# Kernel optimization log

Hardware: AMD Instinct MI355X
Metric: run time of the kernel (lower is better)

Reference implementation:

```python
import jax, jax.numpy as jnp
import numpy as np
import math

PHI = (1 + math.sqrt(5)) / 2
TABLE_SIZE = 4096
TWO_PI = 2.0 * math.pi
_ang = np.arange(TABLE_SIZE, dtype=np.float32) * (TWO_PI / TABLE_SIZE)
SIN_T = jnp.asarray(np.sin(_ang))
COS_T = jnp.asarray(np.cos(_ang))


def lookup_sin_cos(theta):
    """LUT sin/cos with linear interpolation over a 4096-entry table on [0, 2pi)."""
    pos = (theta / TWO_PI % 1.0) * TABLE_SIZE
    i0f = jnp.floor(pos)
    frac = pos - i0f
    i0 = i0f.astype(jnp.int32) % TABLE_SIZE
    i1 = (i0 + 1) % TABLE_SIZE
    s = SIN_T[i0] * (1.0 - frac) + SIN_T[i1] * frac
    c = COS_T[i0] * (1.0 - frac) + COS_T[i1] * frac
    return s, c


def setup_inputs() -> dict:
    key = jax.random.key(0)
    ks = jax.random.split(key, 8)
    B, S, D, H = 2, 2048, 1024, 16
    dh = D // H
    return {
        "x": jax.random.normal(ks[0], (B, S, D), dtype=jnp.float32),
        "w_q": jax.random.normal(ks[1], (H, dh), dtype=jnp.float32) * 0.02,
        "b_q": jnp.zeros((H, dh), jnp.float32),
        "phi_q": jnp.full((H, dh), PHI, jnp.float32),
        "w_k": jax.random.normal(ks[2], (H, dh), dtype=jnp.float32) * 0.02,
        "b_k": jnp.zeros((H, dh), jnp.float32),
        "phi_k": jnp.full((H, dh), PHI, jnp.float32),
        "w_v": jax.random.normal(ks[3], (H, dh), dtype=jnp.float32) * 0.02,
        "b_v": jnp.zeros((H, dh), jnp.float32),
        "w_out": jax.random.normal(ks[4], (D,), dtype=jnp.float32) * 0.02,
        "b_out": jnp.zeros((D,), jnp.float32),
    }


def reference(x, w_q, b_q, phi_q, w_k, b_k, phi_k, w_v, b_v, w_out, b_out):
    B, S, D = x.shape
    H, dh = w_q.shape
    scale = math.sqrt(2 * dh)
    t = jnp.arange(S, dtype=x.dtype).reshape(1, S, 1, 1)
    xh = x.reshape(B, S, H, dh)

    theta_q = xh / (1.0 + jnp.abs(w_q)) + b_q + t * phi_q
    sin_q, cos_q = lookup_sin_cos(theta_q)
    Q = jnp.concatenate([cos_q, sin_q], axis=-1)  # (B,S,H,2dh)

    theta_k = xh / (1.0 + jnp.abs(w_k)) + b_k + t * phi_k
    sin_k, cos_k = lookup_sin_cos(theta_k)
    K = jnp.concatenate([cos_k, sin_k], axis=-1)  # (B,S,H,2dh)

    theta_v = xh / (1.0 + jnp.abs(w_v)) + b_v
    sin_v, cos_v = lookup_sin_cos(theta_v)
    V = cos_v + sin_v  # (B,S,H,dh)

    scores = jnp.einsum('bqhd,bkhd->bhqk', Q, K) / scale
    causal = jnp.triu(jnp.ones((S, S), dtype=bool), k=1)
    scores = jnp.where(causal, -jnp.inf, scores)
    attn = jax.nn.softmax(scores, axis=-1)
    out = jnp.einsum('bhqk,bkhd->bqhd', attn, V).reshape(B, S, D)

    theta_out = out / (1.0 + jnp.abs(w_out)) + b_out
    sin_o, cos_o = lookup_sin_cos(theta_out)
    return cos_o + sin_o
```

## Files before the change

### kernel.cpp

```cpp
#include <hip/hip_runtime.h>
#include <hip/hip_bf16.h>
#include <math.h>

#define BB 2
#define SS 2048
#define HH 16
#define DH 64
#define DQK 128
#define DD (HH*DH)
#define QSCALE 0.08838834764831845f

typedef _Float16 half8_t __attribute__((ext_vector_type(8)));
typedef float f32x4_t __attribute__((ext_vector_type(4)));
typedef float f32x4v __attribute__((ext_vector_type(4)));

__device__ __forceinline__ void fsincos(float th, float* sn, float* cs) {
  float rev = th * 0.15915494309189535f;
  rev -= floorf(rev);
  float ang = rev * 6.283185307179586f;
  *sn = __sinf(ang);
  *cs = __cosf(ang);
}

__device__ __forceinline__ void dma16(const void* g, void* l) {
  __builtin_amdgcn_global_load_lds(
      (const __attribute__((address_space(1))) unsigned int*)g,
      (__attribute__((address_space(3))) unsigned int*)l, 16, 0, 0);
}

__global__ __launch_bounds__(256) void gen_qkv(
    const float* __restrict__ x,
    const float* __restrict__ wq, const float* __restrict__ bq,
    const float* __restrict__ phq,
    const float* __restrict__ wk, const float* __restrict__ bk,
    const float* __restrict__ phk,
    const float* __restrict__ wv, const float* __restrict__ bv,
    _Float16* __restrict__ Qd, _Float16* __restrict__ Kd, _Float16* __restrict__ Vtd)
{
  int stile = blockIdx.x & 31;
  int bh    = blockIdx.x >> 5;
  int b = bh >> 4, h = bh & 15;
  int t = threadIdx.x;
  int sl = t >> 2;
  int dq = (t & 3) << 4;
  int s  = stile * 64 + sl;

  __shared__ _Float16 Vl[64 * 65];

  const float* xr = x + (((size_t)b * SS + s) * HH + h) * DH + dq;
  float xv[16];
#pragma unroll
  for (int i = 0; i < 4; i++)
    *(f32x4v*)(&xv[i * 4]) = *(const f32x4v*)(xr + i * 4);

  float tv = (float)s;
  _Float16 qc[16], qs[16], kc[16], ks[16];
#pragma unroll
  for (int i = 0; i < 16; i++) {
    int d = dq + i;
    int hd = h * DH + d;
    {
      float th = xv[i] / (1.f + fabsf(wq[hd])) + bq[hd] + tv * phq[hd];
      float sn, cs; fsincos(th, &sn, &cs);
      qc[i] = (_Float16)(cs * QSCALE);
      qs[i] = (_Float16)(sn * QSCALE);
    }
    {
      float th = xv[i] / (1.f + fabsf(wk[hd])) + bk[hd] + tv * phk[hd];
      float sn, cs; fsincos(th, &sn, &cs);
      kc[i] = (_Float16)cs;
      ks[i] = (_Float16)sn;
    }
    {
      float th = xv[i] / (1.f + fabsf(wv[hd])) + bv[hd];
      float sn, cs; fsincos(th, &sn, &cs);
      Vl[d * 65 + sl] = (_Float16)(cs + sn);
    }
  }
  size_t qbase = ((size_t)bh * SS + s) * DQK;
#pragma unroll
  for (int i = 0; i < 2; i++) {
    *(half8_t*)(Qd + qbase + dq + i * 8)      = *(half8_t*)(&qc[i * 8]);
    *(half8_t*)(Qd + qbase + DH + dq + i * 8) = *(half8_t*)(&qs[i * 8]);
  }
  {
    size_t ktb = ((size_t)bh * 32 + stile) * 8192;
    int fo0 = (t & 3) * 2;
    *(half8_t*)(Kd + ktb + ((size_t)(fo0    ) * 64 + sl) * 8) = *(half8_t*)(&kc[0]);
    *(half8_t*)(Kd + ktb + ((size_t)(fo0 + 1) * 64 + sl) * 8) = *(half8_t*)(&kc[8]);
    *(half8_t*)(Kd + ktb + ((size_t)(fo0 + 8) * 64 + sl) * 8) = *(half8_t*)(&ks[0]);
    *(half8_t*)(Kd + ktb + ((size_t)(fo0 + 9) * 64 + sl) * 8) = *(half8_t*)(&ks[8]);
  }
  __syncthreads();
#pragma unroll
  for (int i = 0; i < 2; i++) {
    int u = t * 2 + i;
    int dv = u & 63, ku = u >> 6;
    _Float16 tmp[8];
#pragma unroll
    for (int jj = 0; jj < 8; jj++) tmp[jj] = Vl[dv * 65 + ku * 8 + jj];
    *(half8_t*)(Vtd + (((size_t)bh * 32 + stile) * 8 + ku) * 512 + dv * 8) =
        *(half8_t*)tmp;
  }
}

__global__ __launch_bounds__(256) void flash_attn(
    const _Float16* __restrict__ Qd, const _Float16* __restrict__ Kd,
    const _Float16* __restrict__ Vtd,
    const float* __restrict__ wout, const float* __restrict__ bout,
    float* __restrict__ out)
{
  int j  = blockIdx.x & 15;
  int bh = blockIdx.x >> 4;
  int wave = threadIdx.x >> 6;
  int lane = threadIdx.x & 63;
  int lm = lane & 15, lq = lane >> 4;
  int qh = wave >> 1;
  int kh = wave & 1;

  __shared__ __align__(16) _Float16 KV[2][12288];
  __shared__ __align__(16) _Float16 Pbuf[4][32 * 36];

  const _Float16* Kg = Kd + (size_t)bh * 32 * 8192;
  const _Float16* Vg = Vtd + (size_t)bh * 32 * 4096;
  _Float16* Pw = &Pbuf[wave][0];

  for (int phase = 0; phase < 2; ++phase) {
    int qt = phase == 0 ? (31 - j) : j;
    int nch = qt + 1;
    int q0 = qt * 64;

    __syncthreads();

    const _Float16* Qb = Qd + ((size_t)bh * SS + q0 + qh * 32) * DQK;
    half8_t aq[2][4];
#pragma unroll
    for (int mt = 0; mt < 2; mt++)
#pragma unroll
      for (int c = 0; c < 4; c++)
        aq[mt][c] = *(const half8_t*)(Qb + (mt * 16 + lm) * DQK + c * 32 + lq * 8);

    f32x4_t o[2][4];
    float l[2][4];
#pragma unroll
    for (int mt = 0; mt < 2; mt++) {
#pragma unroll
      for (int nt4 = 0; nt4 < 4; nt4++) o[mt][nt4] = (f32x4_t){0.f, 0.f, 0.f, 0.f};
#pragma unroll
      for (int r = 0; r < 4; r++) l[mt][r] = 0.f;
    }

    {
#pragma unroll
      for (int i = 0; i < 4; i++)
        dma16(Kg + (size_t)(wave * 4 + i) * 512 + lane * 8, &KV[0][(wave * 4 + i) * 512]);
#pragma unroll
      for (int i = 0; i < 2; i++)
        dma16(Vg + (size_t)(wave * 2 + i) * 512 + lane * 8, &KV[0][8192 + (wave * 2 + i) * 512]);
    }

    for (int kt = 0; kt < nch; ++kt) {
      int bf = kt & 1;
      asm volatile("s_waitcnt vmcnt(0)" ::: "memory");
      __syncthreads();
      if (kt + 1 < nch) {
        int nb = (kt + 1) & 1;
        const _Float16* gK = Kg + (size_t)(kt + 1) * 8192;
        const _Float16* gV = Vg + (size_t)(kt + 1) * 4096;
#pragma unroll
        for (int i = 0; i < 4; i++)
          dma16(gK + (size_t)(wave * 4 + i) * 512 + lane * 8, &KV[nb][(wave * 4 + i) * 512]);
#pragma unroll
        for (int i = 0; i < 2; i++)
          dma16(gV + (size_t)(wave * 2 + i) * 512 + lane * 8, &KV[nb][8192 + (wave * 2 + i) * 512]);
      }

      const _Float16* lK = &KV[bf][0];
      const _Float16* lV = &KV[bf][8192];
      int k0 = kt * 64;

      f32x4_t cS[2][2];
      cS[0][0] = cS[0][1] = cS[1][0] = cS[1][1] = (f32x4_t){0.f, 0.f, 0.f, 0.f};
#pragma unroll
      for (int c = 0; c < 4; c++) {
        int fo = c * 4 + lq;
        half8_t b0 = *(const half8_t*)(lK + ((size_t)fo * 64 + kh * 32 + lm) * 8);
        half8_t b1 = *(const half8_t*)(lK + ((size_t)fo * 64 + kh * 32 + 16 + lm) * 8);
        cS[0][0] = __builtin_amdgcn_mfma_f32_16x16x32_f16(aq[0][c], b0, cS[0][0], 0, 0, 0);
        cS[1][0] = __builtin_amdgcn_mfma_f32_16x16x32_f16(aq[1][c], b0, cS[1][0], 0, 0, 0);
        cS[0][1] = __builtin_amdgcn_mfma_f32_16x16x32_f16(aq[0][c], b1, cS[0][1], 0, 0, 0);
        cS[1][1] = __builtin_amdgcn_mfma_f32_16x16x32_f16(aq[1][c], b1, cS[1][1], 0, 0, 0);
      }

      bool maskit = (kt == nch - 1);
#pragma unroll
      for (int mt = 0; mt < 2; mt++)
#pragma unroll
        for (int nt = 0; nt < 2; nt++)
#pragma unroll
          for (int r = 0; r < 4; r++) {
            float sv = cS[mt][nt][r] - 8.f;
            if (maskit) {
              int qrow = q0 + qh * 32 + mt * 16 + lq * 4 + r;
              int key  = k0 + kh * 32 + nt * 16 + lm;
              if (key > qrow) sv = -1e30f;
            }
            float p = __expf(sv);
            l[mt][r] += p;
            Pw[(mt * 16 + lq * 4 + r) * 36 + nt * 16 + lm] = (_Float16)p;
          }

      half8_t pa0 = *(const half8_t*)(Pw + (lm) * 36 + lq * 8);
      half8_t pa1 = *(const half8_t*)(Pw + (16 + lm) * 36 + lq * 8);
#pragma unroll
      for (int nt4 = 0; nt4 < 4; nt4++) {
        half8_t bv2 = *(const half8_t*)(lV + ((size_t)(kh * 4 + lq) * 64 + nt4 * 16 + lm) * 8);
        o[0][nt4] = __builtin_amdgcn_mfma_f32_16x16x32_f16(pa0, bv2, o[0][nt4], 0, 0, 0);
        o[1][nt4] = __builtin_amdgcn_mfma_f32_16x16x32_f16(pa1, bv2, o[1][nt4], 0, 0, 0);
      }
    }

    __syncthreads();
    float* Of = (float*)&KV[0][0];
    float* Lf = ((float*)&KV[0][0]) + 2 * 32 * 68;
    if (kh == 1) {
#pragma unroll
      for (int mt = 0; mt < 2; mt++)
#pragma unroll
        for (int r = 0; r < 4; r++) {
          int row = qh * 32 + mt * 16 + lq * 4 + r;
          float* dst = Of + (size_t)row * 68;
#pragma unroll
          for (int nt4 = 0; nt4 < 4; nt4++) dst[nt4 * 16 + lm] = o[mt][nt4][r];
          Lf[(size_t)row * 17 + lm] = l[mt][r];
        }
    }
    __syncthreads();
    if (kh == 0) {
      int b = bh >> 4, hh = bh & 15;
#pragma unroll
      for (int mt = 0; mt < 2; mt++)
#pragma unroll
        for (int r = 0; r < 4; r++) {
          int row = qh * 32 + mt * 16 + lq * 4 + r;
          const float* src = Of + (size_t)row * 68;
          float lsum = l[mt][r] + Lf[(size_t)row * 17 + lm];
#pragma unroll
          for (int off = 1; off < 16; off <<= 1) lsum += __shfl_xor(lsum, off);
          float rl = 1.f / lsum;
          int qrow = q0 + row;
#pragma unroll
          for (int nt4 = 0; nt4 < 4; nt4++) {
            float ov = (o[mt][nt4][r] + src[nt4 * 16 + lm]) * rl;
            int dcol = hh * DH + nt4 * 16 + lm;
            float th = ov / (1.f + fabsf(wout[dcol])) + bout[dcol];
            float sn, cs; fsincos(th, &sn, &cs);
            out[((size_t)b * SS + qrow) * DD + dcol] = cs + sn;
          }
        }
    }
  }
}

extern "C" void kernel_launch(void* const* d_in, const int* in_sizes, int n_in,
                              void* d_out, int out_size, void* d_ws, size_t ws_size,
                              hipStream_t stream) {
  (void)in_sizes; (void)n_in; (void)out_size; (void)ws_size;
  const float* x   = (const float*)d_in[0];
  const float* wq  = (const float*)d_in[1];
  const float* bq  = (const float*)d_in[2];
  const float* phq = (const float*)d_in[3];
  const float* wk  = (const float*)d_in[4];
  const float* bk  = (const float*)d_in[5];
  const float* phk = (const float*)d_in[6];
  const float* wv  = (const float*)d_in[7];
  const float* bv  = (const float*)d_in[8];
  const float* wo  = (const float*)d_in[9];
  const float* bo  = (const float*)d_in[10];

  _Float16* Qd  = (_Float16*)d_ws;
  _Float16* Kd  = Qd + (size_t)BB * HH * SS * DQK;
  _Float16* Vtd = Kd + (size_t)BB * HH * SS * DQK;

  gen_qkv<<<BB * HH * (SS / 64), 256, 0, stream>>>(
      x, wq, bq, phq, wk, bk, phk, wv, bv, Qd, Kd, Vtd);
  flash_attn<<<BB * HH * 16, 256, 0, stream>>>(
      Qd, Kd, Vtd, wo, bo, (float*)d_out);
}
```

Measured before the change: 169.0 us.

## Compute transposed scores to keep P in registers, drop LDS P round-trip

Computes S^T = K·Q^T so that each lane's accumulator already holds the P fragment needed as the B operand for a 16x16x16 MFMA against V^T, removing the per-wave LDS staging buffer for P. It also removes the explicit vmcnt wait before the barrier, remaps block indices so consecutive blocks cover different heads, and rewrites the epilogue so all four waves apply the output sincos with coalesced row-wise stores. The trade-off is twice as many smaller MFMAs for PV, and a possible race on the asynchronous LDS DMA now that the vmcnt wait is gone.

New measurement: 146.4 us. 13.4% less time.

```diff
diff --git a/kernel.cpp b/kernel.cpp
--- a/kernel.cpp
+++ b/kernel.cpp
@@ -11,6 +11,7 @@
 #define QSCALE 0.08838834764831845f
 
 typedef _Float16 half8_t __attribute__((ext_vector_type(8)));
+typedef _Float16 half4_t __attribute__((ext_vector_type(4)));
 typedef float f32x4_t __attribute__((ext_vector_type(4)));
 typedef float f32x4v __attribute__((ext_vector_type(4)));
 
@@ -110,8 +111,8 @@
     const float* __restrict__ wout, const float* __restrict__ bout,
     float* __restrict__ out)
 {
-  int j  = blockIdx.x & 15;
-  int bh = blockIdx.x >> 4;
+  int j  = blockIdx.x >> 5;
+  int bh = blockIdx.x & 31;
   int wave = threadIdx.x >> 6;
   int lane = threadIdx.x & 63;
   int lm = lane & 15, lq = lane >> 4;
@@ -119,11 +120,11 @@
   int kh = wave & 1;
 
   __shared__ __align__(16) _Float16 KV[2][12288];
-  __shared__ __align__(16) _Float16 Pbuf[4][32 * 36];
+  __shared__ __align__(16) float Of[64 * 68];
+  __shared__ __align__(16) float Lf[64];
 
   const _Float16* Kg = Kd + (size_t)bh * 32 * 8192;
   const _Float16* Vg = Vtd + (size_t)bh * 32 * 4096;
-  _Float16* Pw = &Pbuf[wave][0];
 
   for (int phase = 0; phase < 2; ++phase) {
     int qt = phase == 0 ? (31 - j) : j;
@@ -135,20 +136,17 @@
     const _Float16* Qb = Qd + ((size_t)bh * SS + q0 + qh * 32) * DQK;
     half8_t aq[2][4];
 #pragma unroll
-    for (int mt = 0; mt < 2; mt++)
+    for (int qtl = 0; qtl < 2; qtl++)
 #pragma unroll
       for (int c = 0; c < 4; c++)
-        aq[mt][c] = *(const half8_t*)(Qb + (mt * 16 + lm) * DQK + c * 32 + lq * 8);
-
-    f32x4_t o[2][4];
-    float l[2][4];
-#pragma unroll
-    for (int mt = 0; mt < 2; mt++) {
-#pragma unroll
-      for (int nt4 = 0; nt4 < 4; nt4++) o[mt][nt4] = (f32x4_t){0.f, 0.f, 0.f, 0.f};
-#pragma unroll
-      for (int r = 0; r < 4; r++) l[mt][r] = 0.f;
-    }
+        aq[qtl][c] = *(const half8_t*)(Qb + (qtl * 16 + lm) * DQK + c * 32 + lq * 8);
+
+    f32x4_t o[4][2];
+    float l[2] = {0.f, 0.f};
+#pragma unroll
+    for (int dt = 0; dt < 4; dt++)
+#pragma unroll
+      for (int qtl = 0; qtl < 2; qtl++) o[dt][qtl] = (f32x4_t){0.f, 0.f, 0.f, 0.f};
 
     {
 #pragma unroll
@@ -161,7 +159,6 @@
 
     for (int kt = 0; kt < nch; ++kt) {
       int bf = kt & 1;
-      asm volatile("s_waitcnt vmcnt(0)" ::: "memory");
       __syncthreads();
       if (kt + 1 < nch) {
         int nb = (kt + 1) & 1;
@@ -179,85 +176,98 @@
       const _Float16* lV = &KV[bf][8192];
       int k0 = kt * 64;
 
-      f32x4_t cS[2][2];
-      cS[0][0] = cS[0][1] = cS[1][0] = cS[1][1] = (f32x4_t){0.f, 0.f, 0.f, 0.f};
+      f32x4_t cST[2][2];
+      cST[0][0] = cST[0][1] = cST[1][0] = cST[1][1] = (f32x4_t){0.f, 0.f, 0.f, 0.f};
 #pragma unroll
       for (int c = 0; c < 4; c++) {
-        int fo = c * 4 + lq;
-        half8_t b0 = *(const half8_t*)(lK + ((size_t)fo * 64 + kh * 32 + lm) * 8);
-        half8_t b1 = *(const half8_t*)(lK + ((size_t)fo * 64 + kh * 32 + 16 + lm) * 8);
-        cS[0][0] = __builtin_amdgcn_mfma_f32_16x16x32_f16(aq[0][c], b0, cS[0][0], 0, 0, 0);
-        cS[1][0] = __builtin_amdgcn_mfma_f32_16x16x32_f16(aq[1][c], b0, cS[1][0], 0, 0, 0);
-        cS[0][1] = __builtin_amdgcn_mfma_f32_16x16x32_f16(aq[0][c], b1, cS[0][1], 0, 0, 0);
-        cS[1][1] = __builtin_amdgcn_mfma_f32_16x16x32_f16(aq[1][c], b1, cS[1][1], 0, 0, 0);
+        half8_t k0f = *(const half8_t*)(lK + ((size_t)(c * 4 + lq) * 64 + kh * 32 + lm) * 8);
+        half8_t k1f = *(const half8_t*)(lK + ((size_t)(c * 4 + lq) * 64 + kh * 32 + 16 + lm) * 8);
+        cST[0][0] = __builtin_amdgcn_mfma_f32_16x16x32_f16(k0f, aq[0][c], cST[0][0], 0, 0, 0);
+        cST[0][1] = __builtin_amdgcn_mfma_f32_16x16x32_f16(k0f, aq[1][c], cST[0][1], 0, 0, 0);
+        cST[1][0] = __builtin_amdgcn_mfma_f32_16x16x32_f16(k1f, aq[0][c], cST[1][0], 0, 0, 0);
+        cST[1][1] = __builtin_amdgcn_mfma_f32_16x16x32_f16(k1f, aq[1][c], cST[1][1], 0, 0, 0);
       }
 
       bool maskit = (kt == nch - 1);
-#pragma unroll
-      for (int mt = 0; mt < 2; mt++)
-#pragma unroll
-        for (int nt = 0; nt < 2; nt++)
+      half4_t pb[2][2];
+#pragma unroll
+      for (int ktl = 0; ktl < 2; ktl++)
+#pragma unroll
+        for (int qtl = 0; qtl < 2; qtl++) {
+          float pf[4];
 #pragma unroll
           for (int r = 0; r < 4; r++) {
-            float sv = cS[mt][nt][r] - 8.f;
+            float sv = cST[ktl][qtl][r] - 8.f;
             if (maskit) {
-              int qrow = q0 + qh * 32 + mt * 16 + lq * 4 + r;
-              int key  = k0 + kh * 32 + nt * 16 + lm;
+              int key  = k0 + kh * 32 + ktl * 16 + lq * 4 + r;
+              int qrow = q0 + qh * 32 + qtl * 16 + lm;
               if (key > qrow) sv = -1e30f;
             }
-            float p = __expf(sv);
-            l[mt][r] += p;
-            Pw[(mt * 16 + lq * 4 + r) * 36 + nt * 16 + lm] = (_Float16)p;
+            pf[r] = __expf(sv);
+            l[qtl] += pf[r];
           }
-
-      half8_t pa0 = *(const half8_t*)(Pw + (lm) * 36 + lq * 8);
-      half8_t pa1 = *(const half8_t*)(Pw + (16 + lm) * 36 + lq * 8);
-#pragma unroll
-      for (int nt4 = 0; nt4 < 4; nt4++) {
-        half8_t bv2 = *(const half8_t*)(lV + ((size_t)(kh * 4 + lq) * 64 + nt4 * 16 + lm) * 8);
-        o[0][nt4] = __builtin_amdgcn_mfma_f32_16x16x32_f16(pa0, bv2, o[0][nt4], 0, 0, 0);
-        o[1][nt4] = __builtin_amdgcn_mfma_f32_16x16x32_f16(pa1, bv2, o[1][nt4], 0, 0, 0);
-      }
-    }
-
-    __syncthreads();
-    float* Of = (float*)&KV[0][0];
-    float* Lf = ((float*)&KV[0][0]) + 2 * 32 * 68;
+          pb[ktl][qtl] = (half4_t){(_Float16)pf[0], (_Float16)pf[1],
+                                   (_Float16)pf[2], (_Float16)pf[3]};
+        }
+
+#pragma unroll
+      for (int dt = 0; dt < 4; dt++)
+#pragma unroll
+        for (int kg = 0; kg < 2; kg++) {
+          half4_t vf = *(const half4_t*)(lV +
+              ((size_t)(kh * 4 + kg * 2 + (lq >> 1)) * 64 + dt * 16 + lm) * 8 + (lq & 1) * 4);
+          o[dt][0] = __builtin_amdgcn_mfma_f32_16x16x16f16(vf, pb[kg][0], o[dt][0], 0, 0, 0);
+          o[dt][1] = __builtin_amdgcn_mfma_f32_16x16x16f16(vf, pb[kg][1], o[dt][1], 0, 0, 0);
+        }
+    }
+
+#pragma unroll
+    for (int qtl = 0; qtl < 2; qtl++) {
+      l[qtl] += __shfl_xor(l[qtl], 16);
+      l[qtl] += __shfl_xor(l[qtl], 32);
+    }
+
+    __syncthreads();
     if (kh == 1) {
 #pragma unroll
-      for (int mt = 0; mt < 2; mt++)
-#pragma unroll
-        for (int r = 0; r < 4; r++) {
-          int row = qh * 32 + mt * 16 + lq * 4 + r;
-          float* dst = Of + (size_t)row * 68;
-#pragma unroll
-          for (int nt4 = 0; nt4 < 4; nt4++) dst[nt4 * 16 + lm] = o[mt][nt4][r];
-          Lf[(size_t)row * 17 + lm] = l[mt][r];
-        }
+      for (int qtl = 0; qtl < 2; qtl++) {
+        int row = qh * 32 + qtl * 16 + lm;
+#pragma unroll
+        for (int dt = 0; dt < 4; dt++)
+#pragma unroll
+          for (int r = 0; r < 4; r++)
+            Of[row * 68 + dt * 16 + lq * 4 + r] = o[dt][qtl][r];
+        if (lq == 0) Lf[row] = l[qtl];
+      }
     }
     __syncthreads();
     if (kh == 0) {
+#pragma unroll
+      for (int qtl = 0; qtl < 2; qtl++) {
+        int row = qh * 32 + qtl * 16 + lm;
+        float rl = 1.f / (l[qtl] + Lf[row]);
+#pragma unroll
+        for (int dt = 0; dt < 4; dt++)
+#pragma unroll
+          for (int r = 0; r < 4; r++) {
+            int idx = row * 68 + dt * 16 + lq * 4 + r;
+            Of[idx] = (o[dt][qtl][r] + Of[idx]) * rl;
+          }
+      }
+    }
+    __syncthreads();
+    {
       int b = bh >> 4, hh = bh & 15;
-#pragma unroll
-      for (int mt = 0; mt < 2; mt++)
-#pragma unroll
-        for (int r = 0; r < 4; r++) {
-          int row = qh * 32 + mt * 16 + lq * 4 + r;
-          const float* src = Of + (size_t)row * 68;
-          float lsum = l[mt][r] + Lf[(size_t)row * 17 + lm];
-#pragma unroll
-          for (int off = 1; off < 16; off <<= 1) lsum += __shfl_xor(lsum, off);
-          float rl = 1.f / lsum;
-          int qrow = q0 + row;
-#pragma unroll
-          for (int nt4 = 0; nt4 < 4; nt4++) {
-            float ov = (o[mt][nt4][r] + src[nt4 * 16 + lm]) * rl;
-            int dcol = hh * DH + nt4 * 16 + lm;
-            float th = ov / (1.f + fabsf(wout[dcol])) + bout[dcol];
-            float sn, cs; fsincos(th, &sn, &cs);
-            out[((size_t)b * SS + qrow) * DD + dcol] = cs + sn;
-          }
-        }
+      int dcol = hh * DH + lane;
+      float iw = 1.f / (1.f + fabsf(wout[dcol]));
+      float bo = bout[dcol];
+#pragma unroll
+      for (int rr = 0; rr < 16; rr++) {
+        int row = wave * 16 + rr;
+        float th = Of[row * 68 + lane] * iw + bo;
+        float sn, cs; fsincos(th, &sn, &cs);
+        out[((size_t)b * SS + q0 + row) * DD + dcol] = cs + sn;
+      }
     }
   }
 }
```
